# Optimization experiments

Hardware: AMD Instinct MI355X
Metric: run time of the kernel (lower is better)

## Reference

```python
import jax, jax.numpy as jnp
import numpy as np

D, H_DIM, HEADS = 512, 2048, 8

def rmsnorm(x, w):
    eps = jnp.finfo(x.dtype).eps
    return x * jax.lax.rsqrt(jnp.mean(x * x, axis=-1, keepdims=True) + eps) * w

def setup_inputs() -> dict:
    key = jax.random.key(0)
    ks = jax.random.split(key, 16)
    B, N = 2, 2048
    s_d = 1.0 / np.sqrt(D)
    s_h = 1.0 / np.sqrt(H_DIM)
    inp = {
        "x": jax.random.normal(ks[0], (B, N, D), jnp.float32),
        "DA": jax.random.randint(ks[1], (B, 1, N, N), 0, 2, jnp.int32),
        "Wq": jax.random.normal(ks[2], (D, D), jnp.float32) * s_d,
        "bq": jnp.zeros((D,), jnp.float32),
        "Wk": jax.random.normal(ks[3], (D, D), jnp.float32) * s_d,
        "bk": jnp.zeros((D,), jnp.float32),
        "Wv": jax.random.normal(ks[4], (D, D), jnp.float32) * s_d,
        "bv": jnp.zeros((D,), jnp.float32),
        "W1": jax.random.normal(ks[5], (H_DIM, D), jnp.float32) * s_d,
        "b1": jnp.zeros((H_DIM,), jnp.float32),
        "W2": jax.random.normal(ks[6], (H_DIM, D), jnp.float32) * s_d,
        "b2": jnp.zeros((H_DIM,), jnp.float32),
        "W3": jax.random.normal(ks[7], (D, H_DIM), jnp.float32) * s_h,
        "b3": jnp.zeros((D,), jnp.float32),
        "g1": jnp.ones((D,), jnp.float32),
        "g2": jnp.ones((D,), jnp.float32),
    }
    return inp

def reference(x, DA, Wq, bq, Wk, bk, Wv, bv, W1, b1, W2, b2, W3, b3, g1, g2):
    B, N, _ = x.shape
    hd = D // HEADS  # head_dim = 64
    xn = rmsnorm(x, g1)
    # projections (torch Linear: y = x @ W.T + b), split heads -> [B,H,N,hd]
    def split(t):
        return t.reshape(B, N, HEADS, hd).transpose(0, 2, 1, 3)
    q = split(xn @ Wq.T + bq)
    k = split(xn @ Wk.T + bk)
    v = split(xn @ Wv.T + bv)
    scores = jnp.einsum("bhnd,bhmd->bhnm", q, k) / np.sqrt(hd)
    scores = jnp.where(DA == 0, jnp.asarray(-1e20, scores.dtype), scores)
    attn = jax.nn.softmax(scores, axis=-1)
    o = jnp.einsum("bhnm,bhmd->bhnd", attn, v)
    o = o.transpose(0, 2, 1, 3).reshape(B, N, D)
    h = x + o
    hn = rmsnorm(h, g2)
    x2 = hn @ W1.T + b1
    x3 = hn @ W2.T + b2
    out = h + (jax.nn.silu(x2) * x3) @ W3.T + b3
    return out
```

## Files before the change

kernel.cpp:

```cpp
#include <hip/hip_runtime.h>

typedef unsigned short u16;
typedef unsigned int   u32;
typedef unsigned long long u64;

using bf16x8 = __attribute__((ext_vector_type(8))) __bf16;
using f32x4  = __attribute__((ext_vector_type(4))) float;
using us8    = __attribute__((ext_vector_type(8))) u16;
using us4v   = __attribute__((ext_vector_type(4))) u16;

#define NB_TOK   4096
#define DD       512
#define HDIM     2048
#define SEQ      2048
#define NHEAD    8
#define EPS_F32  1.1920929e-7f
#define SM_SHIFT 16.0f

__device__ __forceinline__ u16 f32_to_bf16(float f) {
  u32 u = __float_as_uint(f);
  u += 0x7fffu + ((u >> 16) & 1u);
  return (u16)(u >> 16);
}
__device__ __forceinline__ float bf16_to_f32(u16 h) {
  return __uint_as_float(((u32)h) << 16);
}
__device__ __forceinline__ bf16x8 ld_frag(const u16* p) {
  return __builtin_bit_cast(bf16x8, *(const us8*)p);
}
__device__ __forceinline__ void gload_lds16(const void* g, void* l) {
  __builtin_amdgcn_global_load_lds(
      (__attribute__((address_space(1))) void*)(void*)g,
      (__attribute__((address_space(3))) void*)l, 16, 0, 0);
}
__device__ __forceinline__ float qsum16(float v) {
  v += __shfl_xor(v, 1); v += __shfl_xor(v, 2);
  v += __shfl_xor(v, 4); v += __shfl_xor(v, 8);
  return v;
}

__global__ __launch_bounds__(256) void k_convert(
    const float* __restrict__ wq, const float* __restrict__ wk,
    const float* __restrict__ wv, const float* __restrict__ w1,
    const float* __restrict__ w2, const float* __restrict__ w3,
    u16* __restrict__ wqkv, u16* __restrict__ w1b,
    u16* __restrict__ w2b, u16* __restrict__ w3b) {
  int e = (blockIdx.x * 256 + threadIdx.x) * 4;
  const float* src; u16* dst; int off;
  if      (e <  262144) { src = wq; dst = wqkv;          off = e; }
  else if (e <  524288) { src = wk; dst = wqkv + 262144; off = e -  262144; }
  else if (e <  786432) { src = wv; dst = wqkv + 524288; off = e -  524288; }
  else if (e < 1835008) { src = w1; dst = w1b;           off = e -  786432; }
  else if (e < 2883584) { src = w2; dst = w2b;           off = e - 1835008; }
  else                  { src = w3; dst = w3b;           off = e - 2883584; }
  float4 v = *(const float4*)(src + off);
  us4v o;
  o[0] = f32_to_bf16(v.x); o[1] = f32_to_bf16(v.y);
  o[2] = f32_to_bf16(v.z); o[3] = f32_to_bf16(v.w);
  *(us4v*)(dst + off) = o;
}

__global__ __launch_bounds__(256) void k_maskpack(const int* __restrict__ da,
                                                  u64* __restrict__ maskT) {
  int lane = threadIdx.x & 63, wave = threadIdx.x >> 6;
  int row = blockIdx.x * 4 + wave;
  int b = row >> 11, r = row & 2047;
  const int* src = da + (size_t)row * SEQ;
  #pragma unroll 4
  for (int w = 0; w < 32; ++w) {
    int d = src[w * 64 + lane];
    u64 bal = __ballot(d != 0);
    if (lane == 0) maskT[((size_t)(b * 32 + w)) * SEQ + r] = bal;
  }
}

__global__ __launch_bounds__(256) void k_rms1(const float* __restrict__ x,
                                              const float* __restrict__ g1,
                                              u16* __restrict__ xn) {
  int lane = threadIdx.x & 63, wave = threadIdx.x >> 6;
  int row = blockIdx.x * 4 + wave;
  size_t base = (size_t)row * DD + lane * 8;
  float4 a = *(const float4*)(x + base);
  float4 b = *(const float4*)(x + base + 4);
  float ss = a.x*a.x + a.y*a.y + a.z*a.z + a.w*a.w
           + b.x*b.x + b.y*b.y + b.z*b.z + b.w*b.w;
  #pragma unroll
  for (int m = 1; m < 64; m <<= 1) ss += __shfl_xor(ss, m);
  float sc = rsqrtf(ss * (1.0f / DD) + EPS_F32);
  float4 ga = *(const float4*)(g1 + lane * 8);
  float4 gb = *(const float4*)(g1 + lane * 8 + 4);
  us8 o;
  o[0] = f32_to_bf16(a.x * sc * ga.x); o[1] = f32_to_bf16(a.y * sc * ga.y);
  o[2] = f32_to_bf16(a.z * sc * ga.z); o[3] = f32_to_bf16(a.w * sc * ga.w);
  o[4] = f32_to_bf16(b.x * sc * gb.x); o[5] = f32_to_bf16(b.y * sc * gb.y);
  o[6] = f32_to_bf16(b.z * sc * gb.z); o[7] = f32_to_bf16(b.w * sc * gb.w);
  *(us8*)(xn + base) = o;
}

template <int NB>
__device__ __forceinline__ void gemm_tile(const u16* __restrict__ A,
                                          const u16* const* Bm, int K,
                                          int mblk, int nblk, int kbeg, int kend,
                                          u16* lA, u16* lB,
                                          f32x4 (*acc)[4][4]) {
  const int tid = threadIdx.x, lane = tid & 63, wave = tid >> 6;
  const int l15 = lane & 15, quad = lane >> 4;
  const int wm = (wave >> 1) * 64, wn = (wave & 1) * 64;
  for (int k0 = kbeg; k0 < kend; k0 += 32) {
    #pragma unroll
    for (int i = 0; i < 2; ++i) {
      int s = wave * 2 + i;
      int row = s * 16 + l15;
      gload_lds16(A + (size_t)(mblk + row) * K + k0 + quad * 8, lA + s * 512);
      #pragma unroll
      for (int bi = 0; bi < NB; ++bi)
        gload_lds16(Bm[bi] + (size_t)(nblk + row) * K + k0 + quad * 8,
                    lB + bi * 4096 + s * 512);
    }
    __syncthreads();
    bf16x8 af[4], bf[NB][4];
    #pragma unroll
    for (int mt = 0; mt < 4; ++mt)
      af[mt] = ld_frag(lA + ((wm >> 4) + mt) * 512 + lane * 8);
    #pragma unroll
    for (int bi = 0; bi < NB; ++bi)
      #pragma unroll
      for (int nt = 0; nt < 4; ++nt)
        bf[bi][nt] = ld_frag(lB + bi * 4096 + ((wn >> 4) + nt) * 512 + lane * 8);
    #pragma unroll
    for (int bi = 0; bi < NB; ++bi)
      #pragma unroll
      for (int mt = 0; mt < 4; ++mt)
        #pragma unroll
        for (int nt = 0; nt < 4; ++nt)
          acc[bi][mt][nt] = __builtin_amdgcn_mfma_f32_16x16x32_bf16(
              af[mt], bf[bi][nt], acc[bi][mt][nt], 0, 0, 0);
    __syncthreads();
  }
}

__global__ __launch_bounds__(256) void k_qkv(const u16* __restrict__ xn,
                                             const u16* __restrict__ wqkv,
                                             const float* __restrict__ bq,
                                             const float* __restrict__ bk,
                                             const float* __restrict__ bv,
                                             u16* __restrict__ qkv) {
  __shared__ u16 lA[4096], lB[4096];
  int z = blockIdx.z;
  const u16* Bp = wqkv + z * (DD * DD);
  const float* bias = (z == 0) ? bq : ((z == 1) ? bk : bv);
  float scale = (z == 0) ? 0.125f : 1.0f;
  u16* out = qkv + (size_t)z * NB_TOK * DD;
  int mblk = blockIdx.y * 128, nblk = blockIdx.x * 128;
  f32x4 acc[1][4][4];
  #pragma unroll
  for (int mt = 0; mt < 4; ++mt)
    #pragma unroll
    for (int nt = 0; nt < 4; ++nt) acc[0][mt][nt] = (f32x4)0.0f;
  const u16* Bs[1] = {Bp};
  gemm_tile<1>(xn, Bs, DD, mblk, nblk, 0, DD, lA, lB, acc);
  int lane = threadIdx.x & 63, wave = threadIdx.x >> 6;
  int l15 = lane & 15, quad = lane >> 4;
  int wm = (wave >> 1) * 64, wn = (wave & 1) * 64;
  #pragma unroll
  for (int mt = 0; mt < 4; ++mt)
    #pragma unroll
    for (int nt = 0; nt < 4; ++nt) {
      int n = nblk + wn + nt * 16 + l15;
      float bn = bias[n];
      #pragma unroll
      for (int r = 0; r < 4; ++r) {
        int m = mblk + wm + mt * 16 + quad * 4 + r;
        out[(size_t)m * DD + n] = f32_to_bf16((acc[0][mt][nt][r] + bn) * scale);
      }
    }
}

__global__ __launch_bounds__(256) void k_vtrans(const u16* __restrict__ v,
                                                u16* __restrict__ vT) {
  __shared__ u16 lt[64 * 66];
  int bh = blockIdx.y, b = bh >> 3, h = bh & 7;
  int t0 = blockIdx.x * 64;
  #pragma unroll
  for (int i = 0; i < 4; ++i) {
    int chunk = threadIdx.x + i * 256;
    int r = chunk >> 4, c4 = chunk & 15;
    us4v val = *(const us4v*)(v + (size_t)(b * SEQ + t0 + r) * DD + h * 64 + c4 * 4);
    lt[r * 66 + c4 * 4 + 0] = val[0];
    lt[r * 66 + c4 * 4 + 1] = val[1];
    lt[r * 66 + c4 * 4 + 2] = val[2];
    lt[r * 66 + c4 * 4 + 3] = val[3];
  }
  __syncthreads();
  #pragma unroll
  for (int i = 0; i < 4; ++i) {
    int chunk = threadIdx.x + i * 256;
    int d = chunk >> 4, t4 = chunk & 15;
    us4v o;
    o[0] = lt[(t4 * 4 + 0) * 66 + d];
    o[1] = lt[(t4 * 4 + 1) * 66 + d];
    o[2] = lt[(t4 * 4 + 2) * 66 + d];
    o[3] = lt[(t4 * 4 + 3) * 66 + d];
    *(us4v*)(vT + (size_t)(bh * 64 + d) * SEQ + t0 + t4 * 4) = o;
  }
}

__global__ __launch_bounds__(256) void k_attn(const u16* __restrict__ q,
                                              const u16* __restrict__ k,
                                              const u16* __restrict__ vT,
                                              const u64* __restrict__ maskT,
                                              u16* __restrict__ o) {
  __shared__ u16 lQ[4096], lK[8192], lV[8192], lP[4608];
  int tid = threadIdx.x, lane = tid & 63, wave = tid >> 6;
  int l15 = lane & 15, quad = lane >> 4;
  int bh = blockIdx.y, b = bh >> 3, h = bh & 7;
  int q0 = blockIdx.x * 64;
  const u16* qg = q + (size_t)(b * SEQ + q0) * DD + h * 64;
  const u16* kg = k + (size_t)(b * SEQ) * DD + h * 64;
  const u16* vg = vT + (size_t)bh * 64 * SEQ;
  const u64* mg = maskT + (size_t)b * 32 * SEQ + q0 + wave * 16 + quad * 4;

  #pragma unroll
  for (int i = 0; i < 2; ++i) {
    int s = wave * 2 + i;
    int row = (s >> 1) * 16 + l15, c = (s & 1) * 4 + quad;
    gload_lds16(qg + (size_t)row * DD + c * 8, lQ + s * 512);
    gload_lds16(kg + (size_t)row * DD + c * 8, lK + s * 512);
    gload_lds16(vg + (size_t)row * SEQ + c * 8, lV + s * 512);
  }
  __syncthreads();
  bf16x8 qa[2];
  qa[0] = ld_frag(lQ + wave * 1024 + lane * 8);
  qa[1] = ld_frag(lQ + wave * 1024 + 512 + lane * 8);

  f32x4 oa[4];
  float ls[4];
  #pragma unroll
  for (int r = 0; r < 4; ++r) { oa[r] = (f32x4)0.0f; ls[r] = 0.0f; }

  u16* pw = lP + wave * 1152;

  for (int t = 0; t < 32; ++t) {
    const u16* lKc = lK + (t & 1) * 4096;
    const u16* lVc = lV + (t & 1) * 4096;

    u64 mw[4];
    #pragma unroll
    for (int r = 0; r < 4; ++r) mw[r] = mg[(size_t)t * SEQ + r];

    if (t + 1 < 32) {
      int kv1 = (t + 1) * 64;
      u16* dK = lK + ((t + 1) & 1) * 4096;
      u16* dV = lV + ((t + 1) & 1) * 4096;
      #pragma unroll
      for (int i = 0; i < 2; ++i) {
        int s = wave * 2 + i;
        int row = (s >> 1) * 16 + l15, c = (s & 1) * 4 + quad;
        gload_lds16(kg + (size_t)(kv1 + row) * DD + c * 8, dK + s * 512);
        gload_lds16(vg + (size_t)row * SEQ + kv1 + c * 8, dV + s * 512);
      }
    }

    f32x4 sa[4];
    #pragma unroll
    for (int nt = 0; nt < 4; ++nt) sa[nt] = (f32x4)0.0f;
    #pragma unroll
    for (int ks = 0; ks < 2; ++ks) {
      bf16x8 kb[4];
      #pragma unroll
      for (int nt = 0; nt < 4; ++nt)
        kb[nt] = ld_frag(lKc + nt * 1024 + ks * 512 + lane * 8);
      #pragma unroll
      for (int nt = 0; nt < 4; ++nt)
        sa[nt] = __builtin_amdgcn_mfma_f32_16x16x32_bf16(qa[ks], kb[nt], sa[nt], 0, 0, 0);
    }

    #pragma unroll
    for (int r = 0; r < 4; ++r) {
      u32 mlo = (u32)mw[r], mhi = (u32)(mw[r] >> 32);
      #pragma unroll
      for (int nt = 0; nt < 4; ++nt) {
        u32 word = (nt < 2) ? mlo : mhi;
        u32 bit = (word >> ((nt & 1) * 16 + l15)) & 1u;
        float p = __expf(sa[nt][r] - SM_SHIFT);
        p = bit ? p : 0.0f;
        sa[nt][r] = p;
        ls[r] += p;
      }
    }

    #pragma unroll
    for (int nt = 0; nt < 4; ++nt)
      #pragma unroll
      for (int r = 0; r < 4; ++r)
        pw[(quad * 4 + r) * 72 + nt * 16 + l15] = f32_to_bf16(sa[nt][r]);

    #pragma unroll
    for (int ks = 0; ks < 2; ++ks) {
      bf16x8 pa = ld_frag(pw + l15 * 72 + ks * 32 + quad * 8);
      bf16x8 vb[4];
      #pragma unroll
      for (int dt = 0; dt < 4; ++dt)
        vb[dt] = ld_frag(lVc + dt * 1024 + ks * 512 + lane * 8);
      #pragma unroll
      for (int dt = 0; dt < 4; ++dt)
        oa[dt] = __builtin_amdgcn_mfma_f32_16x16x32_bf16(pa, vb[dt], oa[dt], 0, 0, 0);
    }

    __syncthreads();
  }

  #pragma unroll
  for (int r = 0; r < 4; ++r) {
    float l = qsum16(ls[r]);
    float inv = (l > 0.0f) ? (1.0f / l) : 0.0f;
    int m = q0 + wave * 16 + quad * 4 + r;
    #pragma unroll
    for (int dt = 0; dt < 4; ++dt) {
      int d = dt * 16 + l15;
      o[(size_t)(b * SEQ + m) * DD + h * 64 + d] = f32_to_bf16(oa[dt][r] * inv);
    }
  }
}

__global__ __launch_bounds__(256) void k_rms2(const float* __restrict__ x,
                                              const u16* __restrict__ ob,
                                              const float* __restrict__ b3,
                                              const float* __restrict__ g2,
                                              float* __restrict__ outinit,
                                              u16* __restrict__ hn) {
  int lane = threadIdx.x & 63, wave = threadIdx.x >> 6;
  int row = blockIdx.x * 4 + wave;
  size_t base = (size_t)row * DD + lane * 8;
  float4 a = *(const float4*)(x + base);
  float4 b = *(const float4*)(x + base + 4);
  us8 ov = *(const us8*)(ob + base);
  float hv[8];
  hv[0] = a.x + bf16_to_f32(ov[0]); hv[1] = a.y + bf16_to_f32(ov[1]);
  hv[2] = a.z + bf16_to_f32(ov[2]); hv[3] = a.w + bf16_to_f32(ov[3]);
  hv[4] = b.x + bf16_to_f32(ov[4]); hv[5] = b.y + bf16_to_f32(ov[5]);
  hv[6] = b.z + bf16_to_f32(ov[6]); hv[7] = b.w + bf16_to_f32(ov[7]);
  float ss = 0.0f;
  #pragma unroll
  for (int j = 0; j < 8; ++j) ss += hv[j] * hv[j];
  #pragma unroll
  for (int m = 1; m < 64; m <<= 1) ss += __shfl_xor(ss, m);
  float sc = rsqrtf(ss * (1.0f / DD) + EPS_F32);
  float4 c0 = *(const float4*)(b3 + lane * 8);
  float4 c1 = *(const float4*)(b3 + lane * 8 + 4);
  float4 w0 = {hv[0] + c0.x, hv[1] + c0.y, hv[2] + c0.z, hv[3] + c0.w};
  float4 w1 = {hv[4] + c1.x, hv[5] + c1.y, hv[6] + c1.z, hv[7] + c1.w};
  *(float4*)(outinit + base) = w0;
  *(float4*)(outinit + base + 4) = w1;
  float4 ga = *(const float4*)(g2 + lane * 8);
  float4 gb = *(const float4*)(g2 + lane * 8 + 4);
  us8 hb;
  hb[0] = f32_to_bf16(hv[0] * sc * ga.x); hb[1] = f32_to_bf16(hv[1] * sc * ga.y);
  hb[2] = f32_to_bf16(hv[2] * sc * ga.z); hb[3] = f32_to_bf16(hv[3] * sc * ga.w);
  hb[4] = f32_to_bf16(hv[4] * sc * gb.x); hb[5] = f32_to_bf16(hv[5] * sc * gb.y);
  hb[6] = f32_to_bf16(hv[6] * sc * gb.z); hb[7] = f32_to_bf16(hv[7] * sc * gb.w);
  *(us8*)(hn + base) = hb;
}

__global__ __launch_bounds__(256) void k_ffn12(const u16* __restrict__ hn,
                                               const u16* __restrict__ w1,
                                               const u16* __restrict__ w2,
                                               const float* __restrict__ b1,
                                               const float* __restrict__ b2,
                                               u16* __restrict__ g) {
  __shared__ u16 lA[4096], lB[8192];
  int mblk = blockIdx.y * 128, nblk = blockIdx.x * 128;
  f32x4 acc[2][4][4];
  #pragma unroll
  for (int bi = 0; bi < 2; ++bi)
    #pragma unroll
    for (int mt = 0; mt < 4; ++mt)
      #pragma unroll
      for (int nt = 0; nt < 4; ++nt) acc[bi][mt][nt] = (f32x4)0.0f;
  const u16* Bs[2] = {w1, w2};
  gemm_tile<2>(hn, Bs, DD, mblk, nblk, 0, DD, lA, lB, acc);
  int lane = threadIdx.x & 63, wave = threadIdx.x >> 6;
  int l15 = lane & 15, quad = lane >> 4;
  int wm = (wave >> 1) * 64, wn = (wave & 1) * 64;
  #pragma unroll
  for (int mt = 0; mt < 4; ++mt)
    #pragma unroll
    for (int nt = 0; nt < 4; ++nt) {
      int n = nblk + wn + nt * 16 + l15;
      float bb1 = b1[n], bb2 = b2[n];
      #pragma unroll
      for (int r = 0; r < 4; ++r) {
        int m = mblk + wm + mt * 16 + quad * 4 + r;
        float x2 = acc[0][mt][nt][r] + bb1;
        float x3 = acc[1][mt][nt][r] + bb2;
        float si = x2 / (1.0f + __expf(-x2));
        g[(size_t)m * HDIM + n] = f32_to_bf16(si * x3);
      }
    }
}

__global__ __launch_bounds__(256) void k_ffn3(const u16* __restrict__ g,
                                              const u16* __restrict__ w3,
                                              float* __restrict__ out) {
  __shared__ u16 lA[4096], lB[4096];
  int mblk = blockIdx.y * 128, nblk = blockIdx.x * 128, z = blockIdx.z;
  f32x4 acc[1][4][4];
  #pragma unroll
  for (int mt = 0; mt < 4; ++mt)
    #pragma unroll
    for (int nt = 0; nt < 4; ++nt) acc[0][mt][nt] = (f32x4)0.0f;
  const u16* Bs[1] = {w3};
  gemm_tile<1>(g, Bs, HDIM, mblk, nblk, z * 1024, z * 1024 + 1024, lA, lB, acc);
  int lane = threadIdx.x & 63, wave = threadIdx.x >> 6;
  int l15 = lane & 15, quad = lane >> 4;
  int wm = (wave >> 1) * 64, wn = (wave & 1) * 64;
  #pragma unroll
  for (int mt = 0; mt < 4; ++mt)
    #pragma unroll
    for (int nt = 0; nt < 4; ++nt) {
      int n = nblk + wn + nt * 16 + l15;
      #pragma unroll
      for (int r = 0; r < 4; ++r) {
        int m = mblk + wm + mt * 16 + quad * 4 + r;
        atomicAdd(out + (size_t)m * DD + n, acc[0][mt][nt][r]);
      }
    }
}

#define WS_XN    ((size_t)0)
#define WS_WQKV  ((size_t)4194304)
#define WS_W1B   ((size_t)5767168)
#define WS_W2B   ((size_t)7864320)
#define WS_W3B   ((size_t)9961472)
#define WS_MASK  ((size_t)12058624)
#define WS_QB    ((size_t)28835840)
#define WS_KB    ((size_t)33030144)
#define WS_VB    ((size_t)37224448)
#define WS_VT    ((size_t)41418752)
#define WS_OB    ((size_t)45613056)
#define WS_HN    ((size_t)49807360)
#define WS_G     ((size_t)54001664)

extern "C" void kernel_launch(void* const* d_in, const int* in_sizes, int n_in,
                              void* d_out, int out_size, void* d_ws, size_t ws_size,
                              hipStream_t stream) {
  (void)in_sizes; (void)n_in; (void)out_size; (void)ws_size;
  const float* x  = (const float*)d_in[0];
  const int*   DA = (const int*)d_in[1];
  const float* Wq = (const float*)d_in[2];
  const float* bq = (const float*)d_in[3];
  const float* Wk = (const float*)d_in[4];
  const float* bk = (const float*)d_in[5];
  const float* Wv = (const float*)d_in[6];
  const float* bv = (const float*)d_in[7];
  const float* W1 = (const float*)d_in[8];
  const float* b1 = (const float*)d_in[9];
  const float* W2 = (const float*)d_in[10];
  const float* b2 = (const float*)d_in[11];
  const float* W3 = (const float*)d_in[12];
  const float* b3 = (const float*)d_in[13];
  const float* g1 = (const float*)d_in[14];
  const float* g2 = (const float*)d_in[15];
  float* out = (float*)d_out;
  char* w = (char*)d_ws;

  u16* xn   = (u16*)(w + WS_XN);
  u16* wqkv = (u16*)(w + WS_WQKV);
  u16* w1b  = (u16*)(w + WS_W1B);
  u16* w2b  = (u16*)(w + WS_W2B);
  u16* w3b  = (u16*)(w + WS_W3B);
  u64* mskT = (u64*)(w + WS_MASK);
  u16* qb   = (u16*)(w + WS_QB);
  u16* kb   = (u16*)(w + WS_KB);
  u16* vb   = (u16*)(w + WS_VB);
  u16* vt   = (u16*)(w + WS_VT);
  u16* ob   = (u16*)(w + WS_OB);
  u16* hn   = (u16*)(w + WS_HN);
  u16* gb   = (u16*)(w + WS_G);

  k_convert<<<3840, 256, 0, stream>>>(Wq, Wk, Wv, W1, W2, W3, wqkv, w1b, w2b, w3b);
  k_maskpack<<<1024, 256, 0, stream>>>(DA, mskT);
  k_rms1<<<1024, 256, 0, stream>>>(x, g1, xn);
  k_qkv<<<dim3(4, 32, 3), 256, 0, stream>>>(xn, wqkv, bq, bk, bv, qb);
  k_vtrans<<<dim3(32, 16), 256, 0, stream>>>(vb, vt);
  k_attn<<<dim3(32, 16), 256, 0, stream>>>(qb, kb, vt, mskT, ob);
  k_rms2<<<1024, 256, 0, stream>>>(x, ob, b3, g2, out, hn);
  k_ffn12<<<dim3(16, 32), 256, 0, stream>>>(hn, w1b, w2b, b1, b2, gb);
  k_ffn3<<<dim3(4, 32, 2), 256, 0, stream>>>(gb, w3b, out);
}
```

Baseline: 314.0 us.

## Split attention over KV halves, fuse preprocessing kernels, write V transposed from QKV GEMM

Attention now splits the key/value range in two along a new grid dimension. Each half writes unnormalized fp32 partial outputs and row sums, and the second RMSNorm kernel combines and normalizes them. The aim is to double the number of attention blocks so the GPU is better filled. Weight conversion, mask packing and the first RMSNorm merge into one launch, and the QKV GEMM writes V directly in transposed form, which removes the separate transpose kernel. The S tile is computed transposed (K as the A operand) so packed bf16 probabilities can be stored with 64-bit writes, and the row sum uses the truncated bf16 values. The cost is extra fp32 partial-output traffic through global memory.

```diff
diff --git a/kernel.cpp b/kernel.cpp
--- a/kernel.cpp
+++ b/kernel.cpp
@@ -13,7 +13,6 @@
 #define DD       512
 #define HDIM     2048
 #define SEQ      2048
-#define NHEAD    8
 #define EPS_F32  1.1920929e-7f
 #define SM_SHIFT 16.0f
 
@@ -33,68 +32,62 @@
       (__attribute__((address_space(1))) void*)(void*)g,
       (__attribute__((address_space(3))) void*)l, 16, 0, 0);
 }
-__device__ __forceinline__ float qsum16(float v) {
-  v += __shfl_xor(v, 1); v += __shfl_xor(v, 2);
-  v += __shfl_xor(v, 4); v += __shfl_xor(v, 8);
-  return v;
-}
-
-__global__ __launch_bounds__(256) void k_convert(
+
+__global__ __launch_bounds__(256) void k_pre(
     const float* __restrict__ wq, const float* __restrict__ wk,
     const float* __restrict__ wv, const float* __restrict__ w1,
     const float* __restrict__ w2, const float* __restrict__ w3,
+    const int* __restrict__ da, const float* __restrict__ x,
+    const float* __restrict__ g1,
     u16* __restrict__ wqkv, u16* __restrict__ w1b,
-    u16* __restrict__ w2b, u16* __restrict__ w3b) {
-  int e = (blockIdx.x * 256 + threadIdx.x) * 4;
-  const float* src; u16* dst; int off;
-  if      (e <  262144) { src = wq; dst = wqkv;          off = e; }
-  else if (e <  524288) { src = wk; dst = wqkv + 262144; off = e -  262144; }
-  else if (e <  786432) { src = wv; dst = wqkv + 524288; off = e -  524288; }
-  else if (e < 1835008) { src = w1; dst = w1b;           off = e -  786432; }
-  else if (e < 2883584) { src = w2; dst = w2b;           off = e - 1835008; }
-  else                  { src = w3; dst = w3b;           off = e - 2883584; }
-  float4 v = *(const float4*)(src + off);
-  us4v o;
-  o[0] = f32_to_bf16(v.x); o[1] = f32_to_bf16(v.y);
-  o[2] = f32_to_bf16(v.z); o[3] = f32_to_bf16(v.w);
-  *(us4v*)(dst + off) = o;
-}
-
-__global__ __launch_bounds__(256) void k_maskpack(const int* __restrict__ da,
-                                                  u64* __restrict__ maskT) {
-  int lane = threadIdx.x & 63, wave = threadIdx.x >> 6;
-  int row = blockIdx.x * 4 + wave;
-  int b = row >> 11, r = row & 2047;
-  const int* src = da + (size_t)row * SEQ;
-  #pragma unroll 4
-  for (int w = 0; w < 32; ++w) {
-    int d = src[w * 64 + lane];
-    u64 bal = __ballot(d != 0);
-    if (lane == 0) maskT[((size_t)(b * 32 + w)) * SEQ + r] = bal;
-  }
-}
-
-__global__ __launch_bounds__(256) void k_rms1(const float* __restrict__ x,
-                                              const float* __restrict__ g1,
-                                              u16* __restrict__ xn) {
-  int lane = threadIdx.x & 63, wave = threadIdx.x >> 6;
-  int row = blockIdx.x * 4 + wave;
-  size_t base = (size_t)row * DD + lane * 8;
-  float4 a = *(const float4*)(x + base);
-  float4 b = *(const float4*)(x + base + 4);
-  float ss = a.x*a.x + a.y*a.y + a.z*a.z + a.w*a.w
-           + b.x*b.x + b.y*b.y + b.z*b.z + b.w*b.w;
-  #pragma unroll
-  for (int m = 1; m < 64; m <<= 1) ss += __shfl_xor(ss, m);
-  float sc = rsqrtf(ss * (1.0f / DD) + EPS_F32);
-  float4 ga = *(const float4*)(g1 + lane * 8);
-  float4 gb = *(const float4*)(g1 + lane * 8 + 4);
-  us8 o;
-  o[0] = f32_to_bf16(a.x * sc * ga.x); o[1] = f32_to_bf16(a.y * sc * ga.y);
-  o[2] = f32_to_bf16(a.z * sc * ga.z); o[3] = f32_to_bf16(a.w * sc * ga.w);
-  o[4] = f32_to_bf16(b.x * sc * gb.x); o[5] = f32_to_bf16(b.y * sc * gb.y);
-  o[6] = f32_to_bf16(b.z * sc * gb.z); o[7] = f32_to_bf16(b.w * sc * gb.w);
-  *(us8*)(xn + base) = o;
+    u16* __restrict__ w2b, u16* __restrict__ w3b,
+    u64* __restrict__ maskT, u16* __restrict__ xn) {
+  int bx = blockIdx.x;
+  if (bx < 3840) {
+    int e = (bx * 256 + threadIdx.x) * 4;
+    const float* src; u16* dst; int off;
+    if      (e <  262144) { src = wq; dst = wqkv;          off = e; }
+    else if (e <  524288) { src = wk; dst = wqkv + 262144; off = e -  262144; }
+    else if (e <  786432) { src = wv; dst = wqkv + 524288; off = e -  524288; }
+    else if (e < 1835008) { src = w1; dst = w1b;           off = e -  786432; }
+    else if (e < 2883584) { src = w2; dst = w2b;           off = e - 1835008; }
+    else                  { src = w3; dst = w3b;           off = e - 2883584; }
+    float4 v = *(const float4*)(src + off);
+    us4v o;
+    o[0] = f32_to_bf16(v.x); o[1] = f32_to_bf16(v.y);
+    o[2] = f32_to_bf16(v.z); o[3] = f32_to_bf16(v.w);
+    *(us4v*)(dst + off) = o;
+  } else if (bx < 4864) {
+    int lane = threadIdx.x & 63, wave = threadIdx.x >> 6;
+    int row = (bx - 3840) * 4 + wave;
+    int b = row >> 11, r = row & 2047;
+    const int* src = da + (size_t)row * SEQ;
+    #pragma unroll 4
+    for (int w = 0; w < 32; ++w) {
+      int d = src[w * 64 + lane];
+      u64 bal = __ballot(d != 0);
+      if (lane == 0) maskT[((size_t)(b * 32 + w)) * SEQ + r] = bal;
+    }
+  } else {
+    int lane = threadIdx.x & 63, wave = threadIdx.x >> 6;
+    int row = (bx - 4864) * 4 + wave;
+    size_t base = (size_t)row * DD + lane * 8;
+    float4 a = *(const float4*)(x + base);
+    float4 b = *(const float4*)(x + base + 4);
+    float ss = a.x*a.x + a.y*a.y + a.z*a.z + a.w*a.w
+             + b.x*b.x + b.y*b.y + b.z*b.z + b.w*b.w;
+    #pragma unroll
+    for (int m = 1; m < 64; m <<= 1) ss += __shfl_xor(ss, m);
+    float sc = rsqrtf(ss * (1.0f / DD) + EPS_F32);
+    float4 ga = *(const float4*)(g1 + lane * 8);
+    float4 gb = *(const float4*)(g1 + lane * 8 + 4);
+    us8 o;
+    o[0] = f32_to_bf16(a.x * sc * ga.x); o[1] = f32_to_bf16(a.y * sc * ga.y);
+    o[2] = f32_to_bf16(a.z * sc * ga.z); o[3] = f32_to_bf16(a.w * sc * ga.w);
+    o[4] = f32_to_bf16(b.x * sc * gb.x); o[5] = f32_to_bf16(b.y * sc * gb.y);
+    o[6] = f32_to_bf16(b.z * sc * gb.z); o[7] = f32_to_bf16(b.w * sc * gb.w);
+    *(us8*)(xn + base) = o;
+  }
 }
 
 template <int NB>
@@ -144,13 +137,14 @@
                                              const float* __restrict__ bq,
                                              const float* __restrict__ bk,
                                              const float* __restrict__ bv,
-                                             u16* __restrict__ qkv) {
+                                             u16* __restrict__ qb,
+                                             u16* __restrict__ kb,
+                                             u16* __restrict__ vt) {
   __shared__ u16 lA[4096], lB[4096];
   int z = blockIdx.z;
   const u16* Bp = wqkv + z * (DD * DD);
   const float* bias = (z == 0) ? bq : ((z == 1) ? bk : bv);
   float scale = (z == 0) ? 0.125f : 1.0f;
-  u16* out = qkv + (size_t)z * NB_TOK * DD;
   int mblk = blockIdx.y * 128, nblk = blockIdx.x * 128;
   f32x4 acc[1][4][4];
   #pragma unroll
@@ -162,46 +156,34 @@
   int lane = threadIdx.x & 63, wave = threadIdx.x >> 6;
   int l15 = lane & 15, quad = lane >> 4;
   int wm = (wave >> 1) * 64, wn = (wave & 1) * 64;
-  #pragma unroll
-  for (int mt = 0; mt < 4; ++mt)
-    #pragma unroll
-    for (int nt = 0; nt < 4; ++nt) {
-      int n = nblk + wn + nt * 16 + l15;
-      float bn = bias[n];
-      #pragma unroll
-      for (int r = 0; r < 4; ++r) {
-        int m = mblk + wm + mt * 16 + quad * 4 + r;
-        out[(size_t)m * DD + n] = f32_to_bf16((acc[0][mt][nt][r] + bn) * scale);
-      }
-    }
-}
-
-__global__ __launch_bounds__(256) void k_vtrans(const u16* __restrict__ v,
-                                                u16* __restrict__ vT) {
-  __shared__ u16 lt[64 * 66];
-  int bh = blockIdx.y, b = bh >> 3, h = bh & 7;
-  int t0 = blockIdx.x * 64;
-  #pragma unroll
-  for (int i = 0; i < 4; ++i) {
-    int chunk = threadIdx.x + i * 256;
-    int r = chunk >> 4, c4 = chunk & 15;
-    us4v val = *(const us4v*)(v + (size_t)(b * SEQ + t0 + r) * DD + h * 64 + c4 * 4);
-    lt[r * 66 + c4 * 4 + 0] = val[0];
-    lt[r * 66 + c4 * 4 + 1] = val[1];
-    lt[r * 66 + c4 * 4 + 2] = val[2];
-    lt[r * 66 + c4 * 4 + 3] = val[3];
-  }
-  __syncthreads();
-  #pragma unroll
-  for (int i = 0; i < 4; ++i) {
-    int chunk = threadIdx.x + i * 256;
-    int d = chunk >> 4, t4 = chunk & 15;
-    us4v o;
-    o[0] = lt[(t4 * 4 + 0) * 66 + d];
-    o[1] = lt[(t4 * 4 + 1) * 66 + d];
-    o[2] = lt[(t4 * 4 + 2) * 66 + d];
-    o[3] = lt[(t4 * 4 + 3) * 66 + d];
-    *(us4v*)(vT + (size_t)(bh * 64 + d) * SEQ + t0 + t4 * 4) = o;
+  if (z < 2) {
+    u16* out = z ? kb : qb;
+    #pragma unroll
+    for (int mt = 0; mt < 4; ++mt)
+      #pragma unroll
+      for (int nt = 0; nt < 4; ++nt) {
+        int n = nblk + wn + nt * 16 + l15;
+        float bn = bias[n];
+        #pragma unroll
+        for (int r = 0; r < 4; ++r) {
+          int m = mblk + wm + mt * 16 + quad * 4 + r;
+          out[(size_t)m * DD + n] = f32_to_bf16((acc[0][mt][nt][r] + bn) * scale);
+        }
+      }
+  } else {
+    #pragma unroll
+    for (int mt = 0; mt < 4; ++mt)
+      #pragma unroll
+      for (int nt = 0; nt < 4; ++nt) {
+        int n = nblk + wn + nt * 16 + l15;
+        float bn = bias[n];
+        int m = mblk + wm + mt * 16 + quad * 4;
+        int b = m >> 11, tok = m & 2047;
+        us4v o;
+        #pragma unroll
+        for (int r = 0; r < 4; ++r) o[r] = f32_to_bf16(acc[0][mt][nt][r] + bn);
+        *(us4v*)(vt + ((size_t)(b * 8 + (n >> 6)) * 64 + (n & 63)) * SEQ + tok) = o;
+      }
   }
 }
 
@@ -209,16 +191,19 @@
                                               const u16* __restrict__ k,
                                               const u16* __restrict__ vT,
                                               const u64* __restrict__ maskT,
-                                              u16* __restrict__ o) {
-  __shared__ u16 lQ[4096], lK[8192], lV[8192], lP[4608];
+                                              float* __restrict__ Opart,
+                                              float* __restrict__ lpart) {
+  __shared__ u16 lQ[4096], lK[8192], lV[8192], lP[4 * 16 * 72];
   int tid = threadIdx.x, lane = tid & 63, wave = tid >> 6;
   int l15 = lane & 15, quad = lane >> 4;
   int bh = blockIdx.y, b = bh >> 3, h = bh & 7;
   int q0 = blockIdx.x * 64;
+  int z = blockIdx.z;
+  int kvbase = z * 1024;
   const u16* qg = q + (size_t)(b * SEQ + q0) * DD + h * 64;
-  const u16* kg = k + (size_t)(b * SEQ) * DD + h * 64;
-  const u16* vg = vT + (size_t)bh * 64 * SEQ;
-  const u64* mg = maskT + (size_t)b * 32 * SEQ + q0 + wave * 16 + quad * 4;
+  const u16* kg = k + (size_t)(b * SEQ + kvbase) * DD + h * 64;
+  const u16* vg = vT + (size_t)bh * 64 * SEQ + kvbase;
+  const u64* mg = maskT + ((size_t)(b * 32 + z * 16)) * SEQ + q0 + wave * 16 + l15;
 
   #pragma unroll
   for (int i = 0; i < 2; ++i) {
@@ -234,21 +219,20 @@
   qa[1] = ld_frag(lQ + wave * 1024 + 512 + lane * 8);
 
   f32x4 oa[4];
-  float ls[4];
-  #pragma unroll
-  for (int r = 0; r < 4; ++r) { oa[r] = (f32x4)0.0f; ls[r] = 0.0f; }
+  #pragma unroll
+  for (int r = 0; r < 4; ++r) oa[r] = (f32x4)0.0f;
+  float ls = 0.0f;
 
   u16* pw = lP + wave * 1152;
 
-  for (int t = 0; t < 32; ++t) {
+  for (int t = 0; t < 16; ++t) {
     const u16* lKc = lK + (t & 1) * 4096;
     const u16* lVc = lV + (t & 1) * 4096;
 
-    u64 mw[4];
-    #pragma unroll
-    for (int r = 0; r < 4; ++r) mw[r] = mg[(size_t)t * SEQ + r];
-
-    if (t + 1 < 32) {
+    u64 mw = mg[(size_t)t * SEQ];
+    u64 mq = mw >> (quad * 4);
+
+    if (t + 1 < 16) {
       int kv1 = (t + 1) * 64;
       u16* dK = lK + ((t + 1) & 1) * 4096;
       u16* dV = lV + ((t + 1) & 1) * 4096;
@@ -263,37 +247,35 @@
 
     f32x4 sa[4];
     #pragma unroll
-    for (int nt = 0; nt < 4; ++nt) sa[nt] = (f32x4)0.0f;
+    for (int mt = 0; mt < 4; ++mt) sa[mt] = (f32x4)0.0f;
     #pragma unroll
     for (int ks = 0; ks < 2; ++ks) {
-      bf16x8 kb[4];
-      #pragma unroll
-      for (int nt = 0; nt < 4; ++nt)
-        kb[nt] = ld_frag(lKc + nt * 1024 + ks * 512 + lane * 8);
-      #pragma unroll
-      for (int nt = 0; nt < 4; ++nt)
-        sa[nt] = __builtin_amdgcn_mfma_f32_16x16x32_bf16(qa[ks], kb[nt], sa[nt], 0, 0, 0);
-    }
-
-    #pragma unroll
-    for (int r = 0; r < 4; ++r) {
-      u32 mlo = (u32)mw[r], mhi = (u32)(mw[r] >> 32);
-      #pragma unroll
-      for (int nt = 0; nt < 4; ++nt) {
-        u32 word = (nt < 2) ? mlo : mhi;
-        u32 bit = (word >> ((nt & 1) * 16 + l15)) & 1u;
-        float p = __expf(sa[nt][r] - SM_SHIFT);
-        p = bit ? p : 0.0f;
-        sa[nt][r] = p;
-        ls[r] += p;
-      }
-    }
-
-    #pragma unroll
-    for (int nt = 0; nt < 4; ++nt)
-      #pragma unroll
-      for (int r = 0; r < 4; ++r)
-        pw[(quad * 4 + r) * 72 + nt * 16 + l15] = f32_to_bf16(sa[nt][r]);
+      bf16x8 ka[4];
+      #pragma unroll
+      for (int mt = 0; mt < 4; ++mt)
+        ka[mt] = ld_frag(lKc + (mt * 2 + ks) * 512 + lane * 8);
+      #pragma unroll
+      for (int mt = 0; mt < 4; ++mt)
+        sa[mt] = __builtin_amdgcn_mfma_f32_16x16x32_bf16(ka[mt], qa[ks], sa[mt], 0, 0, 0);
+    }
+
+    #pragma unroll
+    for (int mt = 0; mt < 4; ++mt) {
+      u32 nib = (u32)(mq >> (mt * 16)) & 0xFu;
+      u32 pb[4];
+      #pragma unroll
+      for (int r = 0; r < 4; ++r) {
+        float p = __expf(sa[mt][r] - SM_SHIFT);
+        p = (nib >> r) & 1u ? p : 0.0f;
+        u32 ub = __float_as_uint(p) & 0xffff0000u;
+        ls += __uint_as_float(ub);
+        pb[r] = ub;
+      }
+      u32 lo = __builtin_amdgcn_perm(pb[1], pb[0], 0x07060302u);
+      u32 hi = __builtin_amdgcn_perm(pb[3], pb[2], 0x07060302u);
+      u64 pk = ((u64)hi << 32) | lo;
+      *(u64*)(pw + l15 * 72 + mt * 16 + quad * 4) = pk;
+    }
 
     #pragma unroll
     for (int ks = 0; ks < 2; ++ks) {
@@ -301,7 +283,7 @@
       bf16x8 vb[4];
       #pragma unroll
       for (int dt = 0; dt < 4; ++dt)
-        vb[dt] = ld_frag(lVc + dt * 1024 + ks * 512 + lane * 8);
+        vb[dt] = ld_frag(lVc + (dt * 2 + ks) * 512 + lane * 8);
       #pragma unroll
       for (int dt = 0; dt < 4; ++dt)
         oa[dt] = __builtin_amdgcn_mfma_f32_16x16x32_bf16(pa, vb[dt], oa[dt], 0, 0, 0);
@@ -310,36 +292,52 @@
     __syncthreads();
   }
 
+  ls += __shfl_xor(ls, 16);
+  ls += __shfl_xor(ls, 32);
+  if (quad == 0)
+    lpart[((size_t)z * 16 + bh) * SEQ + q0 + wave * 16 + l15] = ls;
+
+  float* Og = Opart + (size_t)z * NB_TOK * DD;
   #pragma unroll
   for (int r = 0; r < 4; ++r) {
-    float l = qsum16(ls[r]);
-    float inv = (l > 0.0f) ? (1.0f / l) : 0.0f;
     int m = q0 + wave * 16 + quad * 4 + r;
-    #pragma unroll
-    for (int dt = 0; dt < 4; ++dt) {
-      int d = dt * 16 + l15;
-      o[(size_t)(b * SEQ + m) * DD + h * 64 + d] = f32_to_bf16(oa[dt][r] * inv);
-    }
+    float* dst = Og + (size_t)(b * SEQ + m) * DD + h * 64;
+    #pragma unroll
+    for (int dt = 0; dt < 4; ++dt)
+      dst[dt * 16 + l15] = oa[dt][r];
   }
 }
 
 __global__ __launch_bounds__(256) void k_rms2(const float* __restrict__ x,
-                                              const u16* __restrict__ ob,
+                                              const float* __restrict__ Opart,
+                                              const float* __restrict__ lpart,
                                               const float* __restrict__ b3,
                                               const float* __restrict__ g2,
                                               float* __restrict__ outinit,
                                               u16* __restrict__ hn) {
   int lane = threadIdx.x & 63, wave = threadIdx.x >> 6;
   int row = blockIdx.x * 4 + wave;
+  int b = row >> 11, tok = row & 2047, hh = lane >> 3;
   size_t base = (size_t)row * DD + lane * 8;
+  float l0 = lpart[(size_t)(b * 8 + hh) * SEQ + tok];
+  float l1 = lpart[(size_t)(16 + b * 8 + hh) * SEQ + tok];
+  float lsum = l0 + l1;
+  float inv = (lsum > 0.0f) ? (1.0f / lsum) : 0.0f;
   float4 a = *(const float4*)(x + base);
-  float4 b = *(const float4*)(x + base + 4);
-  us8 ov = *(const us8*)(ob + base);
+  float4 bb = *(const float4*)(x + base + 4);
+  float4 o0a = *(const float4*)(Opart + base);
+  float4 o0b = *(const float4*)(Opart + base + 4);
+  float4 o1a = *(const float4*)(Opart + (size_t)NB_TOK * DD + base);
+  float4 o1b = *(const float4*)(Opart + (size_t)NB_TOK * DD + base + 4);
   float hv[8];
-  hv[0] = a.x + bf16_to_f32(ov[0]); hv[1] = a.y + bf16_to_f32(ov[1]);
-  hv[2] = a.z + bf16_to_f32(ov[2]); hv[3] = a.w + bf16_to_f32(ov[3]);
-  hv[4] = b.x + bf16_to_f32(ov[4]); hv[5] = b.y + bf16_to_f32(ov[5]);
-  hv[6] = b.z + bf16_to_f32(ov[6]); hv[7] = b.w + bf16_to_f32(ov[7]);
+  hv[0] = a.x  + (o0a.x + o1a.x) * inv;
+  hv[1] = a.y  + (o0a.y + o1a.y) * inv;
+  hv[2] = a.z  + (o0a.z + o1a.z) * inv;
+  hv[3] = a.w  + (o0a.w + o1a.w) * inv;
+  hv[4] = bb.x + (o0b.x + o1b.x) * inv;
+  hv[5] = bb.y + (o0b.y + o1b.y) * inv;
+  hv[6] = bb.z + (o0b.z + o1b.z) * inv;
+  hv[7] = bb.w + (o0b.w + o1b.w) * inv;
   float ss = 0.0f;
   #pragma unroll
   for (int j = 0; j < 8; ++j) ss += hv[j] * hv[j];
@@ -427,19 +425,20 @@
     }
 }
 
-#define WS_XN    ((size_t)0)
-#define WS_WQKV  ((size_t)4194304)
-#define WS_W1B   ((size_t)5767168)
-#define WS_W2B   ((size_t)7864320)
-#define WS_W3B   ((size_t)9961472)
-#define WS_MASK  ((size_t)12058624)
-#define WS_QB    ((size_t)28835840)
-#define WS_KB    ((size_t)33030144)
-#define WS_VB    ((size_t)37224448)
-#define WS_VT    ((size_t)41418752)
-#define WS_OB    ((size_t)45613056)
-#define WS_HN    ((size_t)49807360)
-#define WS_G     ((size_t)54001664)
+#define MB(x) ((size_t)(x) * 1048576)
+#define WS_XN    MB(0)
+#define WS_WQKV  MB(4)
+#define WS_W1B   MB(6)
+#define WS_W2B   MB(8)
+#define WS_W3B   MB(10)
+#define WS_MASK  MB(12)
+#define WS_QB    MB(16)
+#define WS_KB    MB(20)
+#define WS_VT    MB(24)
+#define WS_OP    MB(28)
+#define WS_LP    MB(44)
+#define WS_HN    MB(45)
+#define WS_G     MB(49)
 
 extern "C" void kernel_launch(void* const* d_in, const int* in_sizes, int n_in,
                               void* d_out, int out_size, void* d_ws, size_t ws_size,
@@ -472,19 +471,17 @@
   u64* mskT = (u64*)(w + WS_MASK);
   u16* qb   = (u16*)(w + WS_QB);
   u16* kb   = (u16*)(w + WS_KB);
-  u16* vb   = (u16*)(w + WS_VB);
   u16* vt   = (u16*)(w + WS_VT);
-  u16* ob   = (u16*)(w + WS_OB);
+  float* Op = (float*)(w + WS_OP);
+  float* lp = (float*)(w + WS_LP);
   u16* hn   = (u16*)(w + WS_HN);
   u16* gb   = (u16*)(w + WS_G);
 
-  k_convert<<<3840, 256, 0, stream>>>(Wq, Wk, Wv, W1, W2, W3, wqkv, w1b, w2b, w3b);
-  k_maskpack<<<1024, 256, 0, stream>>>(DA, mskT);
-  k_rms1<<<1024, 256, 0, stream>>>(x, g1, xn);
-  k_qkv<<<dim3(4, 32, 3), 256, 0, stream>>>(xn, wqkv, bq, bk, bv, qb);
-  k_vtrans<<<dim3(32, 16), 256, 0, stream>>>(vb, vt);
-  k_attn<<<dim3(32, 16), 256, 0, stream>>>(qb, kb, vt, mskT, ob);
-  k_rms2<<<1024, 256, 0, stream>>>(x, ob, b3, g2, out, hn);
+  k_pre<<<5888, 256, 0, stream>>>(Wq, Wk, Wv, W1, W2, W3, DA, x, g1,
+                                  wqkv, w1b, w2b, w3b, mskT, xn);
+  k_qkv<<<dim3(4, 32, 3), 256, 0, stream>>>(xn, wqkv, bq, bk, bv, qb, kb, vt);
+  k_attn<<<dim3(32, 16, 2), 256, 0, stream>>>(qb, kb, vt, mskT, Op, lp);
+  k_rms2<<<1024, 256, 0, stream>>>(x, Op, lp, b3, g2, out, hn);
   k_ffn12<<<dim3(16, 32), 256, 0, stream>>>(hn, w1b, w2b, b1, b2, gb);
   k_ffn3<<<dim3(4, 32, 2), 256, 0, stream>>>(gb, w3b, out);
 }
```

Measured after the change: 299.0 us. 1.05x faster.
